# Kernel tuning notes

Measured on AMD Instinct MI355X. Metric: run time of the kernel, lower is better.

Reference implementation:

```python
import jax, jax.numpy as jnp
import numpy as np

N, CIN, T, V = 16, 16, 512, 200
K, COUT, H = 3, 64, 64


def setup_inputs() -> dict:
    key = jax.random.key(0)
    ks = jax.random.split(key, 9)
    s = 0.05
    return {
        "x": jax.random.normal(ks[0], (N, CIN, T, V), jnp.float32),
        "A": jax.random.uniform(ks[1], (K, V, V), jnp.float32) / V,
        "W_gcn": jax.random.normal(ks[2], (K * COUT, CIN), jnp.float32) * s,
        "b_gcn": jnp.zeros((K * COUT,), jnp.float32),
        "W_ih": jax.random.normal(ks[3], (4 * H, COUT), jnp.float32) * s,
        "W_hh": jax.random.normal(ks[4], (4 * H, H), jnp.float32) * s,
        "b_ih": jnp.zeros((4 * H,), jnp.float32),
        "b_hh": jnp.zeros((4 * H,), jnp.float32),
        "W_fc": jax.random.normal(ks[5], (1, H), jnp.float32) * s,
        "b_fc": jnp.zeros((1,), jnp.float32),
    }


def reference(x, A, W_gcn, b_gcn, W_ih, W_hh, b_ih, b_hh, W_fc, b_fc):
    n, c, t, v = x.shape
    k = A.shape[0]
    cout = W_gcn.shape[0] // k
    # ConvTemporalGraphical: 1x1 conv -> (n, k*cout, t, v), reshape, adjacency einsum
    y = jnp.einsum('nctv,oc->notv', x, W_gcn) + b_gcn[None, :, None, None]
    y = y.reshape(n, k, cout, t, v)
    y = jnp.einsum('nkctv,kvw->nctw', y, A)  # (n, cout, t, v)
    # mean over node dim, residual=False -> res=0
    y = jnp.mean(y, axis=3)  # (n, cout, t)
    seq = jnp.transpose(y, (2, 0, 1))  # (t, n, cout) time-major for scan

    def step(carry, xt):
        h, ccell = carry
        gates = xt @ W_ih.T + b_ih + h @ W_hh.T + b_hh  # (n, 4H)
        i, f, g, o = jnp.split(gates, 4, axis=-1)  # torch LSTM gate order
        i = jax.nn.sigmoid(i)
        f = jax.nn.sigmoid(f)
        g = jnp.tanh(g)
        o = jax.nn.sigmoid(o)
        ccell = f * ccell + i * g
        h = o * jnp.tanh(ccell)
        return (h, ccell), None

    h0 = jnp.zeros((n, W_hh.shape[1]), x.dtype)
    (h_last, _), _ = jax.lax.scan(step, (h0, h0), seq)
    out = h_last @ W_fc.T + b_fc  # (n, 1)
    return (out, A)
```

## Files before the change

### kernel.cpp

```cpp
#include <hip/hip_runtime.h>
#include <math.h>

#define N_    16
#define CIN_  16
#define T_    512
#define V_    200
#define K_    3
#define COUT_ 64
#define H_    64
#define G_    256

#define WS_A  0
#define WS_SA 640
#define WS_XA 1024
#define WS_XW (WS_XA + N_ * T_ * K_ * CIN_)

__device__ __forceinline__ float fast_sig(float x) {
    return __builtin_amdgcn_rcpf(1.f + __expf(-x));
}
__device__ __forceinline__ float fast_tanh(float x) {
    return fmaf(-2.f, __builtin_amdgcn_rcpf(1.f + __expf(2.f * x)), 1.f);
}

#define NCOPY ((K_ * V_ * V_ + 255) / 256)
__global__ __launch_bounds__(256) void prep_kernel(const float* __restrict__ A,
                                                   float* __restrict__ out,
                                                   float* __restrict__ ws) {
    int b = blockIdx.x;
    if (b < NCOPY) {
        int tid = b * 256 + threadIdx.x;
        if (tid < K_ * V_ * V_) out[16 + tid] = A[tid];
        if (tid < K_ * V_) {
            const float* row = A + (long)tid * V_;
            float s = 0.f;
            for (int w = 0; w < V_; ++w) s += row[w];
            ws[WS_A + tid] = s * (1.0f / V_);
        }
    } else {
        int k = b - NCOPY;
        const float* Ak = A + (long)k * V_ * V_;
        float s = 0.f;
        for (int i = threadIdx.x; i < V_ * V_; i += 256) s += Ak[i];
        #pragma unroll
        for (int m = 1; m < 64; m <<= 1) s += __shfl_xor(s, m);
        __shared__ float red[4];
        if ((threadIdx.x & 63) == 0) red[threadIdx.x >> 6] = s;
        __syncthreads();
        if (threadIdx.x == 0)
            ws[WS_SA + k] = (red[0] + red[1] + red[2] + red[3]) * (1.0f / V_);
    }
}

__global__ __launch_bounds__(256) void xa_kernel(const float* __restrict__ x,
                                                 float* __restrict__ ws) {
    __shared__ float aS[K_ * V_];
    int tid = threadIdx.x;
    for (int i = tid; i < K_ * V_; i += 256) aS[i] = ws[WS_A + i];
    __syncthreads();

    int wave = tid >> 6, lane = tid & 63;
    int row = blockIdx.x * 4 + wave;
    const float* xr = x + (long)row * V_;

    float s0 = 0.f, s1 = 0.f, s2 = 0.f;
    for (int v = lane; v < V_; v += 64) {
        float xv = xr[v];
        s0 = fmaf(xv, aS[v], s0);
        s1 = fmaf(xv, aS[V_ + v], s1);
        s2 = fmaf(xv, aS[2 * V_ + v], s2);
    }
    #pragma unroll
    for (int m = 1; m < 64; m <<= 1) {
        s0 += __shfl_xor(s0, m);
        s1 += __shfl_xor(s1, m);
        s2 += __shfl_xor(s2, m);
    }
    if (lane == 0) {
        int t  = row % T_;
        int nc = row / T_;
        int ci = nc % CIN_;
        int n  = nc / CIN_;
        long base = (long)(n * T_ + t) * (K_ * CIN_);
        ws[WS_XA + base + 0 * CIN_ + ci] = s0;
        ws[WS_XA + base + 1 * CIN_ + ci] = s1;
        ws[WS_XA + base + 2 * CIN_ + ci] = s2;
    }
}

__global__ __launch_bounds__(256) void seqgates_kernel(
    const float* __restrict__ W_gcn, const float* __restrict__ b_gcn,
    const float* __restrict__ W_ih, const float* __restrict__ b_ih,
    const float* __restrict__ b_hh, float* __restrict__ ws) {
    int t = blockIdx.x;
    int tid = threadIdx.x;
    __shared__ float xaS[N_][K_ * CIN_];
    __shared__ __align__(16) float seqS[N_][COUT_];
    __shared__ float saS[K_];

    if (tid < K_) saS[tid] = ws[WS_SA + tid];
    #pragma unroll
    for (int r = 0; r < 3; ++r) {
        int i = tid + r * 256;
        if (i < N_ * K_ * CIN_) {
            int n = i / (K_ * CIN_), kc = i % (K_ * CIN_);
            xaS[n][kc] = ws[WS_XA + (long)(n * T_ + t) * (K_ * CIN_) + kc];
        }
    }
    __syncthreads();

    {
        int n = tid >> 4, c0 = (tid & 15) * 4;
        #pragma unroll
        for (int cc = 0; cc < 4; ++cc) {
            int c = c0 + cc;
            float s = 0.f;
            #pragma unroll
            for (int k = 0; k < K_; ++k) {
                s = fmaf(b_gcn[k * COUT_ + c], saS[k], s);
                const float* wrow = W_gcn + (long)(k * COUT_ + c) * CIN_;
                #pragma unroll
                for (int ci = 0; ci < CIN_; ++ci)
                    s = fmaf(wrow[ci], xaS[n][k * CIN_ + ci], s);
            }
            seqS[n][c] = s;
        }
    }
    __syncthreads();

    {
        int g = tid;
        float acc[N_];
        #pragma unroll
        for (int n = 0; n < N_; ++n) acc[n] = 0.f;
        const float4* wrow4 = (const float4*)(W_ih + (long)g * H_);
        #pragma unroll
        for (int c4 = 0; c4 < H_ / 4; ++c4) {
            float4 w4 = wrow4[c4];
            #pragma unroll
            for (int n = 0; n < N_; ++n) {
                float4 s4 = ((const float4*)seqS[n])[c4];
                acc[n] = fmaf(w4.x, s4.x, acc[n]);
                acc[n] = fmaf(w4.y, s4.y, acc[n]);
                acc[n] = fmaf(w4.z, s4.z, acc[n]);
                acc[n] = fmaf(w4.w, s4.w, acc[n]);
            }
        }
        float bias = b_ih[g] + b_hh[g];
        #pragma unroll
        for (int n = 0; n < N_; ++n)
            ws[WS_XW + (long)(t * N_ + n) * G_ + g] = acc[n] + bias;
    }
}

__global__ __launch_bounds__(256, 1) void lstm_kernel(
    const float* __restrict__ W_hh, const float* __restrict__ W_fc,
    const float* __restrict__ b_fc, const float* __restrict__ ws,
    float* __restrict__ out) {
    int n = blockIdx.x;
    int w = threadIdx.x >> 6;
    int lane = threadIdx.x & 63;

    const float4* wr = (const float4*)(W_hh + (long)(w * H_ + lane) * H_);
    float4 w0  = wr[0],  w1  = wr[1],  w2  = wr[2],  w3  = wr[3];
    float4 w4  = wr[4],  w5  = wr[5],  w6  = wr[6],  w7  = wr[7];
    float4 w8  = wr[8],  w9  = wr[9],  w10 = wr[10], w11 = wr[11];
    float4 w12 = wr[12], w13 = wr[13], w14 = wr[14], w15 = wr[15];

    __shared__ __align__(16) float hS[H_];
    __shared__ float gbuf[4][H_];

    if (threadIdx.x < H_) hS[threadIdx.x] = 0.f;
    float ccell = 0.f, hlast = 0.f;
    __syncthreads();

    const float* xw = ws + WS_XW + (long)n * G_ + (w * H_ + lane);
    float x0 = xw[0];
    float x1 = xw[(long)N_ * G_];

    for (int t = 0; t < T_; ++t) {
        float gate = x0;
        x0 = x1;
        if (t + 2 < T_) x1 = xw[(long)(t + 2) * N_ * G_];

        float a0 = 0.f, a1 = 0.f, a2 = 0.f, a3 = 0.f;
        const float4* h4 = (const float4*)hS;
        #define DOT4(i)                          \
            {                                    \
                float4 hv = h4[i];               \
                a0 = fmaf(w##i.x, hv.x, a0);     \
                a1 = fmaf(w##i.y, hv.y, a1);     \
                a2 = fmaf(w##i.z, hv.z, a2);     \
                a3 = fmaf(w##i.w, hv.w, a3);     \
            }
        DOT4(0)  DOT4(1)  DOT4(2)  DOT4(3)
        DOT4(4)  DOT4(5)  DOT4(6)  DOT4(7)
        DOT4(8)  DOT4(9)  DOT4(10) DOT4(11)
        DOT4(12) DOT4(13) DOT4(14) DOT4(15)
        #undef DOT4
        gate += (a0 + a1) + (a2 + a3);

        gbuf[w][lane] = gate;
        __syncthreads();
        if (w == 0) {
            float iv = fast_sig(gate);
            float fv = fast_sig(gbuf[1][lane]);
            float gv = fast_tanh(gbuf[2][lane]);
            float ov = fast_sig(gbuf[3][lane]);
            ccell = fmaf(fv, ccell, iv * gv);
            hlast = ov * fast_tanh(ccell);
            hS[lane] = hlast;
        }
        __syncthreads();
    }

    if (w == 0) {
        float p = hlast * W_fc[lane];
        #pragma unroll
        for (int m = 1; m < 64; m <<= 1) p += __shfl_xor(p, m);
        if (lane == 0) out[n] = p + b_fc[0];
    }
}

extern "C" void kernel_launch(void* const* d_in, const int* in_sizes, int n_in,
                              void* d_out, int out_size, void* d_ws, size_t ws_size,
                              hipStream_t stream) {
    const float* x     = (const float*)d_in[0];
    const float* A     = (const float*)d_in[1];
    const float* W_gcn = (const float*)d_in[2];
    const float* b_gcn = (const float*)d_in[3];
    const float* W_ih  = (const float*)d_in[4];
    const float* W_hh  = (const float*)d_in[5];
    const float* b_ih  = (const float*)d_in[6];
    const float* b_hh  = (const float*)d_in[7];
    const float* W_fc  = (const float*)d_in[8];
    const float* b_fc  = (const float*)d_in[9];
    float* out = (float*)d_out;
    float* ws  = (float*)d_ws;

    prep_kernel<<<NCOPY + K_, 256, 0, stream>>>(A, out, ws);
    int rows = N_ * CIN_ * T_;
    xa_kernel<<<rows / 4, 256, 0, stream>>>(x, ws);
    seqgates_kernel<<<T_, 256, 0, stream>>>(W_gcn, b_gcn, W_ih, b_ih, b_hh, ws);
    lstm_kernel<<<N_, 256, 0, stream>>>(W_hh, W_fc, b_fc, ws, out);
}
```

Before: 385.9 us.

## Stage x tiles in LDS and compute node reductions per thread in xa_kernel

```diff
diff --git a/kernel.cpp b/kernel.cpp
--- a/kernel.cpp
+++ b/kernel.cpp
@@ -51,39 +51,47 @@
     }
 }
 
+#define TT 64
+#define PADV 204
 __global__ __launch_bounds__(256) void xa_kernel(const float* __restrict__ x,
                                                  float* __restrict__ ws) {
-    __shared__ float aS[K_ * V_];
+    __shared__ __align__(16) float xt[TT * PADV];
+    __shared__ __align__(16) float aS[K_ * V_];
     int tid = threadIdx.x;
+    int b = blockIdx.x;
+    int tchunk = b & 7;
+    int ci = (b >> 3) & 15;
+    int n = b >> 7;
+    int t0 = tchunk * TT;
+
     for (int i = tid; i < K_ * V_; i += 256) aS[i] = ws[WS_A + i];
-    __syncthreads();
-
-    int wave = tid >> 6, lane = tid & 63;
-    int row = blockIdx.x * 4 + wave;
-    const float* xr = x + (long)row * V_;
-
-    float s0 = 0.f, s1 = 0.f, s2 = 0.f;
-    for (int v = lane; v < V_; v += 64) {
-        float xv = xr[v];
-        s0 = fmaf(xv, aS[v], s0);
-        s1 = fmaf(xv, aS[V_ + v], s1);
-        s2 = fmaf(xv, aS[2 * V_ + v], s2);
-    }
-    #pragma unroll
-    for (int m = 1; m < 64; m <<= 1) {
-        s0 += __shfl_xor(s0, m);
-        s1 += __shfl_xor(s1, m);
-        s2 += __shfl_xor(s2, m);
-    }
-    if (lane == 0) {
-        int t  = row % T_;
-        int nc = row / T_;
-        int ci = nc % CIN_;
-        int n  = nc / CIN_;
-        long base = (long)(n * T_ + t) * (K_ * CIN_);
-        ws[WS_XA + base + 0 * CIN_ + ci] = s0;
-        ws[WS_XA + base + 1 * CIN_ + ci] = s1;
-        ws[WS_XA + base + 2 * CIN_ + ci] = s2;
+
+    const float4* xg4 =
+        (const float4*)(x + ((long)(n * CIN_ + ci) * T_ + t0) * V_);
+    for (int j = tid; j < TT * (V_ / 4); j += 256) {
+        float4 v = xg4[j];
+        int t = j / (V_ / 4), v4 = (j % (V_ / 4)) * 4;
+        *(float4*)(xt + t * PADV + v4) = v;
+    }
+    __syncthreads();
+
+    int t_local = tid & 63;
+    int k = tid >> 6;
+    if (k < K_) {
+        const float* xr = xt + t_local * PADV;
+        const float* ar = aS + k * V_;
+        float a0 = 0.f, a1 = 0.f, a2 = 0.f, a3 = 0.f;
+        #pragma unroll 5
+        for (int v4 = 0; v4 < V_; v4 += 4) {
+            float4 xv = *(const float4*)(xr + v4);
+            float4 av = *(const float4*)(ar + v4);
+            a0 = fmaf(xv.x, av.x, a0);
+            a1 = fmaf(xv.y, av.y, a1);
+            a2 = fmaf(xv.z, av.z, a2);
+            a3 = fmaf(xv.w, av.w, a3);
+        }
+        float s = (a0 + a1) + (a2 + a3);
+        ws[WS_XA + ((long)n * T_ + (t0 + t_local)) * (K_ * CIN_) + k * CIN_ + ci] = s;
     }
 }
 
@@ -238,8 +246,7 @@
     float* ws  = (float*)d_ws;
 
     prep_kernel<<<NCOPY + K_, 256, 0, stream>>>(A, out, ws);
-    int rows = N_ * CIN_ * T_;
-    xa_kernel<<<rows / 4, 256, 0, stream>>>(x, ws);
+    xa_kernel<<<N_ * CIN_ * (T_ / TT), 256, 0, stream>>>(x, ws);
     seqgates_kernel<<<T_, 256, 0, stream>>>(W_gcn, b_gcn, W_ih, b_ih, b_hh, ws);
     lstm_kernel<<<N_, 256, 0, stream>>>(W_hh, W_fc, b_fc, ws, out);
 }
```

Result: faster. 366.6 us (-5.0%).
